# Optimization experiments

Hardware: AMD Instinct MI355X
Metric: run time of the kernel (lower is better)

## Reference

```python
import jax, jax.numpy as jnp
import numpy as np

B, S, H, NH, FF, L, BLK, R = 2, 4096, 768, 12, 3072, 4, 64, 3
NB = S // BLK          # 64 blocks
D = H // NH            # 64 per-head dim
A = 3 + 2 + R          # window(3) + global(2) + random(R) attended blocks
EPS = 1e-12
SCALE = 1.0 / np.sqrt(D).astype(np.float32)


def setup_inputs() -> dict:
    key = jax.random.key(0)
    ks = jax.random.split(key, 12)
    p = lambda k, shp: jax.random.normal(k, shp, jnp.float32) * 0.02
    return {
        "input_ids": jax.random.normal(ks[0], (B, S, 4), jnp.float32),
        "rand_blocks": jax.random.randint(ks[1], (NB, R), 0, NB, jnp.int32),
        "emb_w": p(ks[2], (4, H)), "emb_b": jnp.zeros((H,), jnp.float32),
        "ln1_g": jnp.ones((L, H), jnp.float32), "ln1_b": jnp.zeros((L, H), jnp.float32),
        "wq": p(ks[3], (L, H, H)), "bq": jnp.zeros((L, H), jnp.float32),
        "wk": p(ks[4], (L, H, H)), "bk": jnp.zeros((L, H), jnp.float32),
        "wv": p(ks[5], (L, H, H)), "bv": jnp.zeros((L, H), jnp.float32),
        "wo": p(ks[6], (L, H, H)), "bo": jnp.zeros((L, H), jnp.float32),
        "ln2_g": jnp.ones((L, H), jnp.float32), "ln2_b": jnp.zeros((L, H), jnp.float32),
        "w1": p(ks[7], (L, H, FF)), "b1": jnp.zeros((L, FF), jnp.float32),
        "w2": p(ks[8], (L, FF, H)), "b2": jnp.zeros((L, H), jnp.float32),
        "clf_w": p(ks[9], (H, 4)), "clf_b": jnp.zeros((4,), jnp.float32),
    }


def _ln(x, g, b):
    m = x.mean(-1, keepdims=True)
    v = jnp.var(x, axis=-1, keepdims=True)  # biased var, like torch LayerNorm
    return (x - m) * jax.lax.rsqrt(v + EPS) * g + b


def _attend_idx(rand_blocks):
    # per query block: [i-1, i, i+1] window (edge-clamped), global {0, NB-1}, R random
    ar = jnp.arange(NB)
    win = jnp.stack([jnp.clip(ar - 1, 0, NB - 1), ar, jnp.clip(ar + 1, 0, NB - 1)], 1)
    glb = jnp.broadcast_to(jnp.array([0, NB - 1], jnp.int32), (NB, 2))
    return jnp.concatenate([win.astype(jnp.int32), glb, rand_blocks], 1)  # [NB, A]


def _attn(x, wq, bq, wk, bk, wv, bv, wo, bo, idx):
    def heads(t):  # [B,S,H] -> [B,NH,NB,BLK,D]
        return t.reshape(B, NB, BLK, NH, D).transpose(0, 3, 1, 2, 4)
    q = heads(x @ wq + bq)
    k = heads(x @ wk + bk)
    v = heads(x @ wv + bv)
    kg = k[:, :, idx].reshape(B, NH, NB, A * BLK, D)  # gather attended key blocks
    vg = v[:, :, idx].reshape(B, NH, NB, A * BLK, D)
    s = jnp.einsum('bhnqd,bhnkd->bhnqk', q, kg) * SCALE  # [B,NH,NB,BLK,A*BLK]
    p = jax.nn.softmax(s, axis=-1)
    o = jnp.einsum('bhnqk,bhnkd->bhnqd', p, vg)
    o = o.transpose(0, 2, 3, 1, 4).reshape(B, S, H)
    return o @ wo + bo


def reference(input_ids, rand_blocks, emb_w, emb_b, ln1_g, ln1_b, wq, bq, wk, bk,
              wv, bv, wo, bo, ln2_g, ln2_b, w1, b1, w2, b2, clf_w, clf_b):
    idx = _attend_idx(rand_blocks)
    x = input_ids @ emb_w + emb_b
    for l in range(L):
        h = _ln(x, ln1_g[l], ln1_b[l])
        x = x + _attn(h, wq[l], bq[l], wk[l], bk[l], wv[l], bv[l], wo[l], bo[l], idx)
        h = _ln(x, ln2_g[l], ln2_b[l])
        x = x + (jax.nn.gelu(h @ w1[l] + b1[l], approximate=False) @ w2[l] + b2[l])
    logits = x @ clf_w + clf_b
    return jax.nn.softmax(logits, axis=-1)
```

## Files before the change

kernel.cpp:

```cpp
#include <hip/hip_runtime.h>
#include <math.h>

constexpr int B  = 2;
constexpr int S  = 4096;
constexpr int H  = 768;
constexpr int NH = 12;
constexpr int FF = 3072;
constexpr int L  = 4;
constexpr int R  = 3;
constexpr int NB = 64;
constexpr int AB = 8;
constexpr float SCALE = 0.125f;
constexpr int QKV_N = 3 * H;

constexpr int ROWS = B * S;
constexpr size_t XSZ = (size_t)B * S * H;

typedef short bf16x8 __attribute__((ext_vector_type(8)));
typedef unsigned short u16x8 __attribute__((ext_vector_type(8)));
typedef float f32x4 __attribute__((ext_vector_type(4)));
typedef unsigned short ushort_t;

__device__ __forceinline__ ushort_t f2b(float f) {
  union { float f; unsigned u; } c; c.f = f;
  unsigned r = c.u + 0x7fffu + ((c.u >> 16) & 1u);
  return (ushort_t)(r >> 16);
}

__device__ __forceinline__ void gload16(const void* g, void* l) {
  __builtin_amdgcn_global_load_lds(
      (const __attribute__((address_space(1))) unsigned int*)g,
      (__attribute__((address_space(3))) unsigned int*)l, 16, 0, 0);
}

__global__ __launch_bounds__(256) void embed_kernel(
    const float* __restrict__ ids, const float* __restrict__ w,
    const float* __restrict__ bvec, float* __restrict__ x) {
  int i = blockIdx.x * 256 + threadIdx.x;
  if (i >= (int)XSZ) return;
  int hc = i % H;
  int bs = i / H;
  float s = bvec[hc];
  #pragma unroll
  for (int j = 0; j < 4; ++j) s += ids[bs * 4 + j] * w[j * H + hc];
  x[i] = s;
}

__global__ __launch_bounds__(256) void ln_kernel(
    const float* __restrict__ x, const float* __restrict__ g,
    const float* __restrict__ bvec, ushort_t* __restrict__ out) {
  int row = blockIdx.x;
  const float* xr = x + (size_t)row * H;
  int t = threadIdx.x;
  float v0 = xr[t], v1 = xr[t + 256], v2 = xr[t + 512];
  float s  = v0 + v1 + v2;
  float ss = v0 * v0 + v1 * v1 + v2 * v2;
  for (int off = 1; off < 64; off <<= 1) {
    s  += __shfl_xor(s,  off);
    ss += __shfl_xor(ss, off);
  }
  __shared__ float sm[8];
  int w = t >> 6, lane = t & 63;
  if (lane == 0) { sm[w] = s; sm[4 + w] = ss; }
  __syncthreads();
  s  = sm[0] + sm[1] + sm[2] + sm[3];
  ss = sm[4] + sm[5] + sm[6] + sm[7];
  float mean = s * (1.0f / H);
  float var  = ss * (1.0f / H) - mean * mean;
  float rstd = rsqrtf(var + 1e-12f);
  ushort_t* orow = out + (size_t)row * H;
  orow[t]       = f2b((v0 - mean) * rstd * g[t]       + bvec[t]);
  orow[t + 256] = f2b((v1 - mean) * rstd * g[t + 256] + bvec[t + 256]);
  orow[t + 512] = f2b((v2 - mean) * rstd * g[t + 512] + bvec[t + 512]);
}

__global__ __launch_bounds__(256) void tcvt_kernel(
    const float* __restrict__ in, ushort_t* __restrict__ out,
    int K, int N, size_t inZ, size_t outZ) {
  __shared__ float tile[32][33];
  const float* inz = in + blockIdx.z * inZ;
  ushort_t* outz = out + blockIdx.z * outZ;
  int k0 = blockIdx.y * 32, n0 = blockIdx.x * 32;
  int tx = threadIdx.x & 31, ty = threadIdx.x >> 5;
  #pragma unroll
  for (int i = 0; i < 4; ++i) {
    int kk = ty + i * 8;
    tile[kk][tx] = inz[(size_t)(k0 + kk) * N + n0 + tx];
  }
  __syncthreads();
  #pragma unroll
  for (int i = 0; i < 4; ++i) {
    int nn = ty + i * 8;
    outz[(size_t)(n0 + nn) * K + k0 + tx] = f2b(tile[tx][nn]);
  }
}

__global__ __launch_bounds__(256) void concat_bias_kernel(
    const float* __restrict__ bq, const float* __restrict__ bk,
    const float* __restrict__ bv, float* __restrict__ out) {
  int i = blockIdx.x * 256 + threadIdx.x;
  if (i >= L * QKV_N) return;
  int l = i / QKV_N, c = i % QKV_N;
  float val = (c < H) ? bq[l * H + c] : (c < 2 * H) ? bk[l * H + c - H] : bv[l * H + c - 2 * H];
  out[i] = val;
}

template <int BM, int EPI>
__global__ __launch_bounds__(256, 4) void bgemm(
    const ushort_t* __restrict__ A, const ushort_t* __restrict__ Wt,
    const float* __restrict__ bias, const float* __restrict__ res,
    float* __restrict__ Cf, ushort_t* __restrict__ Cb,
    int M, int N, int K, int ncol) {
  constexpr int LDSB = (BM + 128) * 32;
  constexpr int NLD  = (BM + 128) / 64;
  constexpr int WM   = BM / 32;
  __shared__ ushort_t lds[2 * LDSB];

  const int nwg = (int)gridDim.x;
  const int qq = nwg >> 3, r0 = nwg & 7;
  const int xcd = (int)blockIdx.x & 7, loc = (int)blockIdx.x >> 3;
  const int swz = (xcd < r0 ? xcd * (qq + 1) : r0 * (qq + 1) + (xcd - r0) * qq) + loc;
  const int bm = (swz / ncol) * BM, bn = (swz % ncol) * 128;

  const int t = threadIdx.x;
  const int wid = t >> 6, lane = t & 63;
  const int fcol = lane & 15, fgrp = lane >> 4;
  const int wm = wid >> 1, wn = wid & 1;
  (void)wid; (void)lane;

  const ushort_t* src[NLD];
  int dst[NLD];
  #pragma unroll
  for (int j = 0; j < NLD; ++j) {
    int idx = j * 2048 + t * 8;
    dst[j] = idx;
    int ch = (idx >> 3) & 3;
    int row;
    const ushort_t* base;
    if (idx < BM * 32) { row = idx >> 5;              base = A  + (size_t)(bm + row) * K; }
    else               { row = (idx - BM * 32) >> 5;  base = Wt + (size_t)(bn + row) * K; }
    src[j] = base + ((ch ^ ((row >> 1) & 3)) << 3);
  }

  f32x4 acc[WM][4] = {};

  #pragma unroll
  for (int j = 0; j < NLD; ++j) gload16(src[j], &lds[dst[j]]);
  int kgl = 32;

  const int NT = K >> 5;
  for (int tau = 0; tau < NT; ++tau) {
    const int cur = (tau & 1) * LDSB;
    if (tau < NT - 1) {
      const int nxt = cur ^ LDSB;
      #pragma unroll
      for (int j = 0; j < NLD; ++j) gload16(src[j] + kgl, &lds[nxt + dst[j]]);
      kgl += 32;
      if constexpr (NLD == 4) { asm volatile("s_waitcnt vmcnt(4)" ::: "memory"); }
      else                    { asm volatile("s_waitcnt vmcnt(3)" ::: "memory"); }
    } else {
      asm volatile("s_waitcnt vmcnt(0)" ::: "memory");
    }
    __builtin_amdgcn_sched_barrier(0);
    __builtin_amdgcn_s_barrier();
    __builtin_amdgcn_sched_barrier(0);

    bf16x8 af[WM], bfr[4];
    #pragma unroll
    for (int mi = 0; mi < WM; ++mi) {
      int row = wm * (BM / 2) + mi * 16 + fcol;
      af[mi] = *(const bf16x8*)&lds[cur + row * 32 + ((fgrp ^ ((row >> 1) & 3)) << 3)];
    }
    #pragma unroll
    for (int ni = 0; ni < 4; ++ni) {
      int row = wn * 64 + ni * 16 + fcol;
      bfr[ni] = *(const bf16x8*)&lds[cur + BM * 32 + row * 32 + ((fgrp ^ ((row >> 1) & 3)) << 3)];
    }
    __builtin_amdgcn_s_setprio(1);
    #pragma unroll
    for (int mi = 0; mi < WM; ++mi)
      #pragma unroll
      for (int ni = 0; ni < 4; ++ni)
        acc[mi][ni] = __builtin_amdgcn_mfma_f32_16x16x32_bf16(af[mi], bfr[ni], acc[mi][ni], 0, 0, 0);
    __builtin_amdgcn_s_setprio(0);

    if (tau < NT - 1) {
      __builtin_amdgcn_sched_barrier(0);
      __builtin_amdgcn_s_barrier();
      __builtin_amdgcn_sched_barrier(0);
    }
  }

  #pragma unroll
  for (int mi = 0; mi < WM; ++mi) {
    const int m = bm + wm * (BM / 2) + mi * 16 + fgrp * 4;
    #pragma unroll
    for (int ni = 0; ni < 4; ++ni) {
      const int n = bn + wn * 64 + ni * 16 + fcol;
      const float bb = bias[n];
      #pragma unroll
      for (int r = 0; r < 4; ++r) {
        float val = acc[mi][ni][r] + bb;
        if (EPI == 1) {
          Cf[(size_t)(m + r) * N + n] = val + res[(size_t)(m + r) * N + n];
        } else if (EPI == 2) {
          val = 0.5f * val * (1.0f + erff(val * 0.70710678118654752f));
          Cb[(size_t)(m + r) * N + n] = f2b(val);
        } else {
          Cb[(size_t)(m + r) * N + n] = f2b(val);
        }
      }
    }
  }
}

__global__ __launch_bounds__(256) void attn_mfma(
    const ushort_t* __restrict__ qkv, const int* __restrict__ rb,
    ushort_t* __restrict__ ao) {
  __shared__ ushort_t Ks[64 * 72];
  __shared__ ushort_t Vt[64 * 72];
  __shared__ ushort_t Ps[4][16 * 72];
  const int n = blockIdx.x, hh = blockIdx.y, b = blockIdx.z;
  const int t = threadIdx.x;
  const int wid = t >> 6, lane = t & 63;
  const int fcol = lane & 15, fgrp = lane >> 4;
  const int qr0 = n * 64 + wid * 16;

  bf16x8 qf[2];
  #pragma unroll
  for (int kc = 0; kc < 2; ++kc)
    qf[kc] = *(const bf16x8*)&qkv[((size_t)(b * S) + qr0 + fcol) * QKV_N + hh * 64 + kc * 32 + fgrp * 8];

  f32x4 oacc[4] = {};
  float mrow[4], lrow[4];
  #pragma unroll
  for (int r = 0; r < 4; ++r) { mrow[r] = -1e30f; lrow[r] = 0.f; }

  const int skp = t >> 3;
  const int sdo = (t & 7) * 8;

  for (int a = 0; a < AB; ++a) {
    int kb;
    if      (a == 0) kb = (n > 0) ? n - 1 : 0;
    else if (a == 1) kb = n;
    else if (a == 2) kb = (n < NB - 1) ? n + 1 : NB - 1;
    else if (a == 3) kb = 0;
    else if (a == 4) kb = NB - 1;
    else             kb = rb[n * R + (a - 5)];

    const ushort_t* kbase = qkv + ((size_t)(b * S) + kb * 64) * QKV_N + H + hh * 64;
    const ushort_t* vbase = qkv + ((size_t)(b * S) + kb * 64) * QKV_N + 2 * H + hh * 64;
    #pragma unroll
    for (int i = 0; i < 2; ++i) {
      int kp = skp + i * 32;
      u16x8 kv = *(const u16x8*)&kbase[(size_t)kp * QKV_N + sdo];
      *(u16x8*)&Ks[kp * 72 + sdo] = kv;
      u16x8 vv = *(const u16x8*)&vbase[(size_t)kp * QKV_N + sdo];
      #pragma unroll
      for (int j = 0; j < 8; ++j) Vt[(sdo + j) * 72 + kp] = vv[j];
    }
    __syncthreads();

    f32x4 sacc[4] = {};
    #pragma unroll
    for (int ni = 0; ni < 4; ++ni)
      #pragma unroll
      for (int kc = 0; kc < 2; ++kc) {
        bf16x8 kf = *(const bf16x8*)&Ks[(ni * 16 + fcol) * 72 + kc * 32 + fgrp * 8];
        sacc[ni] = __builtin_amdgcn_mfma_f32_16x16x32_bf16(qf[kc], kf, sacc[ni], 0, 0, 0);
      }

    #pragma unroll
    for (int ni = 0; ni < 4; ++ni)
      #pragma unroll
      for (int r = 0; r < 4; ++r) sacc[ni][r] *= SCALE;
    #pragma unroll
    for (int r = 0; r < 4; ++r) {
      float tm = fmaxf(fmaxf(sacc[0][r], sacc[1][r]), fmaxf(sacc[2][r], sacc[3][r]));
      tm = fmaxf(tm, __shfl_xor(tm, 1));
      tm = fmaxf(tm, __shfl_xor(tm, 2));
      tm = fmaxf(tm, __shfl_xor(tm, 4));
      tm = fmaxf(tm, __shfl_xor(tm, 8));
      float mn = fmaxf(mrow[r], tm);
      float corr = __expf(mrow[r] - mn);
      mrow[r] = mn;
      float rs = 0.f;
      #pragma unroll
      for (int ni = 0; ni < 4; ++ni) {
        float p = __expf(sacc[ni][r] - mn);
        sacc[ni][r] = p;
        rs += p;
      }
      rs += __shfl_xor(rs, 1);
      rs += __shfl_xor(rs, 2);
      rs += __shfl_xor(rs, 4);
      rs += __shfl_xor(rs, 8);
      lrow[r] = lrow[r] * corr + rs;
      #pragma unroll
      for (int ni = 0; ni < 4; ++ni) oacc[ni][r] *= corr;
    }

    __syncthreads();
    #pragma unroll
    for (int ni = 0; ni < 4; ++ni)
      #pragma unroll
      for (int r = 0; r < 4; ++r)
        Ps[wid][(fgrp * 4 + r) * 72 + ni * 16 + fcol] = f2b(sacc[ni][r]);
    __syncthreads();

    #pragma unroll
    for (int kc = 0; kc < 2; ++kc) {
      bf16x8 pa = *(const bf16x8*)&Ps[wid][fcol * 72 + kc * 32 + fgrp * 8];
      #pragma unroll
      for (int ni = 0; ni < 4; ++ni) {
        bf16x8 vb = *(const bf16x8*)&Vt[(ni * 16 + fcol) * 72 + kc * 32 + fgrp * 8];
        oacc[ni] = __builtin_amdgcn_mfma_f32_16x16x32_bf16(pa, vb, oacc[ni], 0, 0, 0);
      }
    }
    __syncthreads();
  }

  #pragma unroll
  for (int r = 0; r < 4; ++r) {
    float inv = 1.0f / lrow[r];
    int row = qr0 + fgrp * 4 + r;
    #pragma unroll
    for (int ni = 0; ni < 4; ++ni)
      ao[((size_t)(b * S) + row) * H + hh * 64 + ni * 16 + fcol] = f2b(oacc[ni][r] * inv);
  }
}

__global__ __launch_bounds__(64) void clf_kernel(
    const float* __restrict__ x, const float* __restrict__ w,
    const float* __restrict__ bvec, float* __restrict__ out) {
  int row = blockIdx.x;
  int lane = threadIdx.x;
  const float* xr = x + (size_t)row * H;
  float p0 = 0.f, p1 = 0.f, p2 = 0.f, p3 = 0.f;
  for (int d = lane; d < H; d += 64) {
    float xv = xr[d];
    p0 += xv * w[d * 4 + 0];
    p1 += xv * w[d * 4 + 1];
    p2 += xv * w[d * 4 + 2];
    p3 += xv * w[d * 4 + 3];
  }
  for (int off = 1; off < 64; off <<= 1) {
    p0 += __shfl_xor(p0, off);
    p1 += __shfl_xor(p1, off);
    p2 += __shfl_xor(p2, off);
    p3 += __shfl_xor(p3, off);
  }
  if (lane == 0) {
    float l0 = p0 + bvec[0], l1 = p1 + bvec[1], l2 = p2 + bvec[2], l3 = p3 + bvec[3];
    float mx = fmaxf(fmaxf(l0, l1), fmaxf(l2, l3));
    float e0 = __expf(l0 - mx), e1 = __expf(l1 - mx), e2 = __expf(l2 - mx), e3 = __expf(l3 - mx);
    float inv = 1.0f / (e0 + e1 + e2 + e3);
    out[row * 4 + 0] = e0 * inv;
    out[row * 4 + 1] = e1 * inv;
    out[row * 4 + 2] = e2 * inv;
    out[row * 4 + 3] = e3 * inv;
  }
}

extern "C" void kernel_launch(void* const* d_in, const int* in_sizes, int n_in,
                              void* d_out, int out_size, void* d_ws, size_t ws_size,
                              hipStream_t stream) {
  const float* input_ids = (const float*)d_in[0];
  const int*   rand_bl   = (const int*)  d_in[1];
  const float* emb_w = (const float*)d_in[2];
  const float* emb_b = (const float*)d_in[3];
  const float* ln1_g = (const float*)d_in[4];
  const float* ln1_b = (const float*)d_in[5];
  const float* wq = (const float*)d_in[6];
  const float* bq = (const float*)d_in[7];
  const float* wk = (const float*)d_in[8];
  const float* bk = (const float*)d_in[9];
  const float* wv = (const float*)d_in[10];
  const float* bv = (const float*)d_in[11];
  const float* wo = (const float*)d_in[12];
  const float* bo = (const float*)d_in[13];
  const float* ln2_g = (const float*)d_in[14];
  const float* ln2_b = (const float*)d_in[15];
  const float* w1 = (const float*)d_in[16];
  const float* b1 = (const float*)d_in[17];
  const float* w2 = (const float*)d_in[18];
  const float* b2 = (const float*)d_in[19];
  const float* clf_w = (const float*)d_in[20];
  const float* clf_b = (const float*)d_in[21];

  char* p = (char*)d_ws;
  float*    x    = (float*)p;    p += XSZ * 4;
  ushort_t* h    = (ushort_t*)p; p += XSZ * 2;
  ushort_t* qkv  = (ushort_t*)p; p += (size_t)ROWS * QKV_N * 2;
  ushort_t* ao   = (ushort_t*)p; p += XSZ * 2;
  ushort_t* ff   = qkv;
  ushort_t* qkvT = (ushort_t*)p; p += (size_t)L * QKV_N * H * 2;
  ushort_t* woT  = (ushort_t*)p; p += (size_t)L * H * H * 2;
  ushort_t* w1T  = (ushort_t*)p; p += (size_t)L * H * FF * 2;
  ushort_t* w2T  = (ushort_t*)p; p += (size_t)L * FF * H * 2;
  float*    bqkv = (float*)p;    p += (size_t)L * QKV_N * 4;

  tcvt_kernel<<<dim3(H / 32, H / 32, L), 256, 0, stream>>>(
      wq, qkvT + 0 * H * H, H, H, (size_t)H * H, (size_t)QKV_N * H);
  tcvt_kernel<<<dim3(H / 32, H / 32, L), 256, 0, stream>>>(
      wk, qkvT + 1 * H * H, H, H, (size_t)H * H, (size_t)QKV_N * H);
  tcvt_kernel<<<dim3(H / 32, H / 32, L), 256, 0, stream>>>(
      wv, qkvT + 2 * H * H, H, H, (size_t)H * H, (size_t)QKV_N * H);
  tcvt_kernel<<<dim3(H / 32, H / 32, L), 256, 0, stream>>>(
      wo, woT, H, H, (size_t)H * H, (size_t)H * H);
  tcvt_kernel<<<dim3(FF / 32, H / 32, L), 256, 0, stream>>>(
      w1, w1T, H, FF, (size_t)H * FF, (size_t)H * FF);
  tcvt_kernel<<<dim3(H / 32, FF / 32, L), 256, 0, stream>>>(
      w2, w2T, FF, H, (size_t)FF * H, (size_t)FF * H);
  concat_bias_kernel<<<(L * QKV_N + 255) / 256, 256, 0, stream>>>(bq, bk, bv, bqkv);

  embed_kernel<<<(int)((XSZ + 255) / 256), 256, 0, stream>>>(input_ids, emb_w, emb_b, x);

  for (int l = 0; l < L; ++l) {
    ln_kernel<<<ROWS, 256, 0, stream>>>(x, ln1_g + l * H, ln1_b + l * H, h);

    bgemm<128, 0><<<(ROWS / 128) * (QKV_N / 128), 256, 0, stream>>>(
        h, qkvT + (size_t)l * QKV_N * H, bqkv + l * QKV_N, nullptr,
        nullptr, qkv, ROWS, QKV_N, H, QKV_N / 128);

    attn_mfma<<<dim3(NB, NH, B), 256, 0, stream>>>(qkv, rand_bl, ao);

    bgemm<64, 1><<<(ROWS / 64) * (H / 128), 256, 0, stream>>>(
        ao, woT + (size_t)l * H * H, bo + l * H, x, x, nullptr, ROWS, H, H, H / 128);

    ln_kernel<<<ROWS, 256, 0, stream>>>(x, ln2_g + l * H, ln2_b + l * H, h);

    bgemm<128, 2><<<(ROWS / 128) * (FF / 128), 256, 0, stream>>>(
        h, w1T + (size_t)l * H * FF, b1 + l * FF, nullptr,
        nullptr, ff, ROWS, FF, H, FF / 128);

    bgemm<64, 1><<<(ROWS / 64) * (H / 128), 256, 0, stream>>>(
        ff, w2T + (size_t)l * FF * H, b2 + l * H, x, x, nullptr, ROWS, H, FF, H / 128);
  }

  clf_kernel<<<ROWS, 64, 0, stream>>>(x, clf_w, clf_b, (float*)d_out);
}
```

Before: 1.143 ms.

## Triple-buffer GEMM LDS pipeline and use 128x128 tiles for all projections

The bf16 GEMM moves from double to triple buffering in LDS, so two K-slices are in flight while one is computed, with the vmcnt waits adjusted to match. The BM template parameter is removed and every GEMM, including the output and FFN-down projections, now uses 128x128 tiles. This is meant to hide global-load latency and raise reuse per tile. In exchange it uses more LDS, lowers the occupancy hint from 4 to 3, and halves the grid for the N=768 GEMMs (384 workgroups), which may underfill the GPU.

```diff
diff --git a/kernel.cpp b/kernel.cpp
--- a/kernel.cpp
+++ b/kernel.cpp
@@ -105,59 +105,58 @@
   out[i] = val;
 }
 
-template <int BM, int EPI>
-__global__ __launch_bounds__(256, 4) void bgemm(
+template <int EPI>
+__global__ __launch_bounds__(256, 3) void bgemm(
     const ushort_t* __restrict__ A, const ushort_t* __restrict__ Wt,
     const float* __restrict__ bias, const float* __restrict__ res,
     float* __restrict__ Cf, ushort_t* __restrict__ Cb,
     int M, int N, int K, int ncol) {
-  constexpr int LDSB = (BM + 128) * 32;
-  constexpr int NLD  = (BM + 128) / 64;
-  constexpr int WM   = BM / 32;
-  __shared__ ushort_t lds[2 * LDSB];
+  constexpr int LDSB = 8192;
+  __shared__ ushort_t lds[3 * LDSB];
 
   const int nwg = (int)gridDim.x;
   const int qq = nwg >> 3, r0 = nwg & 7;
   const int xcd = (int)blockIdx.x & 7, loc = (int)blockIdx.x >> 3;
   const int swz = (xcd < r0 ? xcd * (qq + 1) : r0 * (qq + 1) + (xcd - r0) * qq) + loc;
-  const int bm = (swz / ncol) * BM, bn = (swz % ncol) * 128;
+  const int bm = (swz / ncol) * 128, bn = (swz % ncol) * 128;
 
   const int t = threadIdx.x;
   const int wid = t >> 6, lane = t & 63;
   const int fcol = lane & 15, fgrp = lane >> 4;
   const int wm = wid >> 1, wn = wid & 1;
-  (void)wid; (void)lane;
-
-  const ushort_t* src[NLD];
-  int dst[NLD];
-  #pragma unroll
-  for (int j = 0; j < NLD; ++j) {
+
+  const ushort_t* src[4];
+  int dst[4];
+  #pragma unroll
+  for (int j = 0; j < 4; ++j) {
     int idx = j * 2048 + t * 8;
     dst[j] = idx;
     int ch = (idx >> 3) & 3;
     int row;
     const ushort_t* base;
-    if (idx < BM * 32) { row = idx >> 5;              base = A  + (size_t)(bm + row) * K; }
-    else               { row = (idx - BM * 32) >> 5;  base = Wt + (size_t)(bn + row) * K; }
+    if (idx < 4096) { row = idx >> 5;           base = A  + (size_t)(bm + row) * K; }
+    else            { row = (idx - 4096) >> 5;  base = Wt + (size_t)(bn + row) * K; }
     src[j] = base + ((ch ^ ((row >> 1) & 3)) << 3);
   }
 
-  f32x4 acc[WM][4] = {};
-
-  #pragma unroll
-  for (int j = 0; j < NLD; ++j) gload16(src[j], &lds[dst[j]]);
-  int kgl = 32;
-
+  f32x4 acc[4][4] = {};
+
+  #pragma unroll
+  for (int j = 0; j < 4; ++j) gload16(src[j], &lds[dst[j]]);
+  #pragma unroll
+  for (int j = 0; j < 4; ++j) gload16(src[j] + 32, &lds[LDSB + dst[j]]);
+  int kgl = 64;
+
+  int bo0 = 0, bo1 = LDSB, bo2 = 2 * LDSB;
   const int NT = K >> 5;
   for (int tau = 0; tau < NT; ++tau) {
-    const int cur = (tau & 1) * LDSB;
-    if (tau < NT - 1) {
-      const int nxt = cur ^ LDSB;
-      #pragma unroll
-      for (int j = 0; j < NLD; ++j) gload16(src[j] + kgl, &lds[nxt + dst[j]]);
+    if (tau + 2 < NT) {
+      #pragma unroll
+      for (int j = 0; j < 4; ++j) gload16(src[j] + kgl, &lds[bo2 + dst[j]]);
       kgl += 32;
-      if constexpr (NLD == 4) { asm volatile("s_waitcnt vmcnt(4)" ::: "memory"); }
-      else                    { asm volatile("s_waitcnt vmcnt(3)" ::: "memory"); }
+      asm volatile("s_waitcnt vmcnt(8)" ::: "memory");
+    } else if (tau + 2 == NT) {
+      asm volatile("s_waitcnt vmcnt(4)" ::: "memory");
     } else {
       asm volatile("s_waitcnt vmcnt(0)" ::: "memory");
     }
@@ -165,20 +164,20 @@
     __builtin_amdgcn_s_barrier();
     __builtin_amdgcn_sched_barrier(0);
 
-    bf16x8 af[WM], bfr[4];
-    #pragma unroll
-    for (int mi = 0; mi < WM; ++mi) {
-      int row = wm * (BM / 2) + mi * 16 + fcol;
-      af[mi] = *(const bf16x8*)&lds[cur + row * 32 + ((fgrp ^ ((row >> 1) & 3)) << 3)];
+    bf16x8 af[4], bfr[4];
+    #pragma unroll
+    for (int mi = 0; mi < 4; ++mi) {
+      int row = wm * 64 + mi * 16 + fcol;
+      af[mi] = *(const bf16x8*)&lds[bo0 + row * 32 + ((fgrp ^ ((row >> 1) & 3)) << 3)];
     }
     #pragma unroll
     for (int ni = 0; ni < 4; ++ni) {
       int row = wn * 64 + ni * 16 + fcol;
-      bfr[ni] = *(const bf16x8*)&lds[cur + BM * 32 + row * 32 + ((fgrp ^ ((row >> 1) & 3)) << 3)];
+      bfr[ni] = *(const bf16x8*)&lds[bo0 + 4096 + row * 32 + ((fgrp ^ ((row >> 1) & 3)) << 3)];
     }
     __builtin_amdgcn_s_setprio(1);
     #pragma unroll
-    for (int mi = 0; mi < WM; ++mi)
+    for (int mi = 0; mi < 4; ++mi)
       #pragma unroll
       for (int ni = 0; ni < 4; ++ni)
         acc[mi][ni] = __builtin_amdgcn_mfma_f32_16x16x32_bf16(af[mi], bfr[ni], acc[mi][ni], 0, 0, 0);
@@ -189,11 +188,12 @@
       __builtin_amdgcn_s_barrier();
       __builtin_amdgcn_sched_barrier(0);
     }
-  }
-
-  #pragma unroll
-  for (int mi = 0; mi < WM; ++mi) {
-    const int m = bm + wm * (BM / 2) + mi * 16 + fgrp * 4;
+    int tmp = bo0; bo0 = bo1; bo1 = bo2; bo2 = tmp;
+  }
+
+  #pragma unroll
+  for (int mi = 0; mi < 4; ++mi) {
+    const int m = bm + wm * 64 + mi * 16 + fgrp * 4;
     #pragma unroll
     for (int ni = 0; ni < 4; ++ni) {
       const int n = bn + wn * 64 + ni * 16 + fcol;
@@ -419,22 +419,22 @@
   for (int l = 0; l < L; ++l) {
     ln_kernel<<<ROWS, 256, 0, stream>>>(x, ln1_g + l * H, ln1_b + l * H, h);
 
-    bgemm<128, 0><<<(ROWS / 128) * (QKV_N / 128), 256, 0, stream>>>(
+    bgemm<0><<<(ROWS / 128) * (QKV_N / 128), 256, 0, stream>>>(
         h, qkvT + (size_t)l * QKV_N * H, bqkv + l * QKV_N, nullptr,
         nullptr, qkv, ROWS, QKV_N, H, QKV_N / 128);
 
     attn_mfma<<<dim3(NB, NH, B), 256, 0, stream>>>(qkv, rand_bl, ao);
 
-    bgemm<64, 1><<<(ROWS / 64) * (H / 128), 256, 0, stream>>>(
+    bgemm<1><<<(ROWS / 128) * (H / 128), 256, 0, stream>>>(
         ao, woT + (size_t)l * H * H, bo + l * H, x, x, nullptr, ROWS, H, H, H / 128);
 
     ln_kernel<<<ROWS, 256, 0, stream>>>(x, ln2_g + l * H, ln2_b + l * H, h);
 
-    bgemm<128, 2><<<(ROWS / 128) * (FF / 128), 256, 0, stream>>>(
+    bgemm<2><<<(ROWS / 128) * (FF / 128), 256, 0, stream>>>(
         h, w1T + (size_t)l * H * FF, b1 + l * FF, nullptr,
         nullptr, ff, ROWS, FF, H, FF / 128);
 
-    bgemm<64, 1><<<(ROWS / 64) * (H / 128), 256, 0, stream>>>(
+    bgemm<1><<<(ROWS / 128) * (H / 128), 256, 0, stream>>>(
         ff, w2T + (size_t)l * FF * H, b2 + l * H, x, x, nullptr, ROWS, H, FF, H / 128);
   }
 
```

New measurement: 1.075 ms. -6.0%, faster.
